# Performance work log

Hardware: AMD Instinct MI355X
Metric: run time of the kernel (lower is better)

## Reference

```python
import jax, jax.numpy as jnp
import numpy as np

B, N, DIM, HEADS = 1, 4096, 1024, 16
HEAD_DIM = DIM // HEADS
SCALE = HEAD_DIM ** -0.5
GRID = 64  # GRID*GRID == N, power-of-2 Hilbert grid


def _hilbert_d2xy(n, d):
    # standard Hilbert curve distance->(x,y), vectorized in numpy
    rx = np.zeros_like(d)
    ry = np.zeros_like(d)
    x = np.zeros_like(d)
    y = np.zeros_like(d)
    t = d.copy()
    s = 1
    while s < n:
        rx = (t // 2) & 1
        ry = (t ^ rx) & 1
        # rotate
        swap = ry == 0
        flip = swap & (rx == 1)
        x_f = np.where(flip, s - 1 - x, x)
        y_f = np.where(flip, s - 1 - y, y)
        x, y = np.where(swap, y_f, x_f), np.where(swap, x_f, y_f)
        x = x + s * rx
        y = y + s * ry
        t = t // 4
        s *= 2
    return x, y


def _hilbert_indices(n_tokens, grid):
    d = np.arange(n_tokens)
    hx, hy = _hilbert_d2xy(grid, d)
    # token at Hilbert distance d lives at row-major position hy*grid+hx
    return (hy * grid + hx).astype(np.int32)


def setup_inputs() -> dict:
    key = jax.random.key(0)
    k1, k2, k3 = jax.random.split(key, 3)
    x = jax.random.normal(k1, (B, N, DIM), dtype=jnp.float32)
    w_qkv = jax.random.normal(k2, (3 * DIM, DIM), dtype=jnp.float32) * (DIM ** -0.5)
    w_out = jax.random.normal(k3, (DIM, DIM), dtype=jnp.float32) * (DIM ** -0.5)
    indices = jnp.asarray(_hilbert_indices(N, GRID))
    return {"x": x, "w_qkv": w_qkv, "w_out": w_out, "indices": indices}


def reference(x, w_qkv, w_out, indices):
    b, n, c = x.shape
    # qkv projection: nn.Linear -> x @ W^T, reshape to [B,N,3,H,Dh]
    qkv = jnp.einsum("bnc,dc->bnd", x, w_qkv).reshape(b, n, 3, HEADS, HEAD_DIM)
    q, k, v = qkv[:, :, 0], qkv[:, :, 1], qkv[:, :, 2]  # each [B,N,H,Dh]
    # Hilbert gather along sequence
    q = q[:, indices]
    k = k[:, indices]
    v = v[:, indices]
    # full softmax attention per head
    scores = jnp.einsum("bnhd,bmhd->bhnm", q, k) * SCALE
    attn = jax.nn.softmax(scores, axis=-1)
    out = jnp.einsum("bhnm,bmhd->bnhd", attn, v)  # [B,N,H,Dh]
    # scatter back to original order
    inv = jnp.argsort(indices)
    out = out[:, inv].reshape(b, n, c)
    return jnp.einsum("bnc,dc->bnd", out, w_out)
```

## Files before the change

kernel.cpp:

```cpp
#include <hip/hip_runtime.h>
#include <stdint.h>

#define NTOK 4096
#define HD 64
#define DIMC 1024

typedef __attribute__((ext_vector_type(8))) short s16x8;
typedef __attribute__((ext_vector_type(4))) float f32x4;

#if __has_builtin(__builtin_amdgcn_exp2f)
#define EXP2(x) __builtin_amdgcn_exp2f(x)
#else
#define EXP2(x) exp2f(x)
#endif

__device__ inline unsigned short f2bf(float f) {
  union { float f; unsigned u; } v; v.f = f;
  unsigned r = v.u + 0x7FFFu + ((v.u >> 16) & 1u);
  return (unsigned short)(r >> 16);
}

__device__ inline unsigned cvt_pk_bf16(float lo, float hi) {
  unsigned r;
  asm("v_cvt_pk_bf16_f32 %0, %1, %2" : "=v"(r) : "v"(lo), "v"(hi));
  return r;
}

__device__ inline float bf2f(unsigned short u) {
  union { unsigned u; float f; } v; v.u = ((unsigned)u) << 16;
  return v.f;
}

__device__ inline void gld16(const void* g, void* s) {
  __builtin_amdgcn_global_load_lds((const __attribute__((address_space(1))) void*)g,
                                   (__attribute__((address_space(3))) void*)s, 16, 0, 0);
}

#define N4_X   1048576
#define N4_WQ  786432
#define N4_WO  262144
__global__ void cvt_all(const float4* __restrict__ x, const float4* __restrict__ wq,
                        const float4* __restrict__ wo, ushort4* __restrict__ xb,
                        ushort4* __restrict__ wqb, ushort4* __restrict__ wob) {
  int i = blockIdx.x * 256 + threadIdx.x;
  const float4* s; ushort4* d; int off;
  if (i < N4_X) { s = x; d = xb; off = i; }
  else if (i < N4_X + N4_WQ) { s = wq; d = wqb; off = i - N4_X; }
  else { s = wo; d = wob; off = i - (N4_X + N4_WQ); }
  float4 v = s[off];
  ushort4 o;
  o.x = f2bf(v.x); o.y = f2bf(v.y); o.z = f2bf(v.z); o.w = f2bf(v.w);
  d[off] = o;
}

#define QSCALE 0.18033688011112042f
template<int EPI>
__global__ __launch_bounds__(256) void gemm_bt(
    const unsigned short* __restrict__ A,
    const unsigned short* __restrict__ B,
    float* __restrict__ outf,
    unsigned short* __restrict__ qb,
    unsigned short* __restrict__ kb,
    unsigned short* __restrict__ vtb,
    int K, int Nout)
{
  __shared__ unsigned short As[128 * 32];
  __shared__ unsigned short Bs[128 * 32];
  const int t = threadIdx.x;
  const int l = t & 63;
  const int w = t >> 6;
  const int wr = w >> 1, wc = w & 1;
  const int bm = blockIdx.x, bn = blockIdx.y;

  f32x4 acc[4][4];
#pragma unroll
  for (int m = 0; m < 4; ++m)
#pragma unroll
    for (int n = 0; n < 4; ++n)
#pragma unroll
      for (int r = 0; r < 4; ++r) acc[m][n][r] = 0.f;

  for (int kt = 0; kt < K; kt += 32) {
    __syncthreads();
#pragma unroll
    for (int j = 0; j < 2; ++j) {
      const int o = j * 4096 + t * 16;
      const int row = o >> 6;
      const int cole = (o & 63) >> 1;
      gld16(A + (size_t)(bm * 128 + row) * K + kt + cole, (char*)As + o);
      gld16(B + (size_t)(bn * 128 + row) * K + kt + cole, (char*)Bs + o);
    }
    __syncthreads();
    s16x8 af[4], bfr[4];
    const int cb = (l >> 4) * 16;
#pragma unroll
    for (int m = 0; m < 4; ++m)
      af[m] = *(const s16x8*)((const char*)As + (wr * 64 + m * 16 + (l & 15)) * 64 + cb);
#pragma unroll
    for (int n = 0; n < 4; ++n)
      bfr[n] = *(const s16x8*)((const char*)Bs + (wc * 64 + n * 16 + (l & 15)) * 64 + cb);
#pragma unroll
    for (int m = 0; m < 4; ++m)
#pragma unroll
      for (int n = 0; n < 4; ++n)
        acc[m][n] = __builtin_amdgcn_mfma_f32_16x16x32_bf16(af[m], bfr[n], acc[m][n], 0, 0, 0);
  }

#pragma unroll
  for (int m = 0; m < 4; ++m) {
#pragma unroll
    for (int n = 0; n < 4; ++n) {
#pragma unroll
      for (int r = 0; r < 4; ++r) {
        const int gm = bm * 128 + wr * 64 + m * 16 + (l >> 4) * 4 + r;
        const int gn = bn * 128 + wc * 64 + n * 16 + (l & 15);
        const float val = acc[m][n][r];
        if (EPI == 0) {
          const int part = gn >> 10;
          const int h = (gn >> 6) & 15;
          const int dd = gn & 63;
          if (part == 0)      qb[((size_t)h * NTOK + gm) * HD + dd] = f2bf(val * QSCALE);
          else if (part == 1) kb[((size_t)h * NTOK + gm) * HD + dd] = f2bf(val);
          else                vtb[((size_t)h * HD + dd) * NTOK + gm] = f2bf(val);
        } else {
          outf[(size_t)gm * Nout + gn] = val;
        }
      }
    }
  }
}

__global__ __launch_bounds__(128, 4) void fa_split(
    const unsigned short* __restrict__ Q,
    const unsigned short* __restrict__ Kin,
    const unsigned short* __restrict__ Vt,
    unsigned short* __restrict__ Opart,
    float* __restrict__ Lpart)
{
  __shared__ unsigned short Ks[2][32 * 64];
  __shared__ unsigned short Vs[2][64 * 32];

  const int t = threadIdx.x, l = t & 63, w = t >> 6;
  const int g = l >> 4, q = l & 15;
  const int wg = blockIdx.x;
  const int h = wg & 15;
  const int qt = (wg >> 4) & 63;
  const int half = wg >> 10;
  const int q0 = qt * 64 + w * 32;
  const int kbase0 = half * (NTOK / 2);
  const unsigned short* Qh = Q + (size_t)h * NTOK * HD;
  const unsigned short* Kh = Kin + (size_t)h * NTOK * HD;
  const unsigned short* Vh = Vt + (size_t)h * HD * NTOK;

  int offK[2], offV[2];
#pragma unroll
  for (int j = 0; j < 2; ++j) {
    const int o = j * 2048 + t * 16;
    const int rho = o >> 7;
    const int c = o & 127;
    const int n = ((rho & 12) << 1) | ((rho & 16) >> 2) | (rho & 3);
    offK[j] = n * 128 + (c ^ ((rho & 7) << 4));
    const int rv = o >> 6;
    offV[j] = rv * (NTOK * 2) + (o & 63);
  }

  s16x8 qf[2][2];
#pragma unroll
  for (int rb = 0; rb < 2; ++rb)
#pragma unroll
    for (int tq = 0; tq < 2; ++tq)
      qf[rb][tq] = *(const s16x8*)(Qh + (size_t)(q0 + rb * 16 + q) * HD + tq * 32 + g * 8);

  s16x8 ones;
#pragma unroll
  for (int i = 0; i < 8; ++i) ones[i] = (short)0x3F80;

  f32x4 oacc[2][4], lacc[2];
#pragma unroll
  for (int rb = 0; rb < 2; ++rb) {
#pragma unroll
    for (int db = 0; db < 4; ++db)
#pragma unroll
      for (int r = 0; r < 4; ++r) oacc[rb][db][r] = 0.f;
#pragma unroll
    for (int r = 0; r < 4; ++r) lacc[rb][r] = 0.f;
  }

#pragma unroll
  for (int j = 0; j < 2; ++j) {
    const int o = j * 2048 + t * 16;
    gld16((const char*)Kh + (size_t)kbase0 * 128 + offK[j], (char*)Ks[0] + o);
    gld16((const char*)Vh + (size_t)kbase0 * 2 + offV[j], (char*)Vs[0] + o);
  }
  __syncthreads();

  int cur = 0;
  const int NIT = (NTOK / 2) / 32;
  for (int it = 0; it < NIT; ++it) {
    if (it + 1 < NIT) {
      const char* kp = (const char*)Kh + (size_t)(kbase0 + (it + 1) * 32) * 128;
      const char* vp = (const char*)Vh + (size_t)(kbase0 + (it + 1) * 32) * 2;
#pragma unroll
      for (int j = 0; j < 2; ++j) {
        const int o = j * 2048 + t * 16;
        gld16(kp + offK[j], (char*)Ks[cur ^ 1] + o);
        gld16(vp + offV[j], (char*)Vs[cur ^ 1] + o);
      }
    }

    const char* kb = (const char*)Ks[cur];
    const char* vb = (const char*)Vs[cur];

    f32x4 sc[2][2];
    __builtin_amdgcn_s_setprio(1);
#pragma unroll
    for (int kb2 = 0; kb2 < 2; ++kb2) {
      const int row = kb2 * 16 + q;
      const int swz = (row & 7) << 4;
      s16x8 kf0 = *(const s16x8*)(kb + row * 128 + ((g * 16) ^ swz));
      s16x8 kf1 = *(const s16x8*)(kb + row * 128 + ((64 + g * 16) ^ swz));
#pragma unroll
      for (int rb = 0; rb < 2; ++rb) {
        f32x4 z = {0.f, 0.f, 0.f, 0.f};
        z = __builtin_amdgcn_mfma_f32_16x16x32_bf16(kf0, qf[rb][0], z, 0, 0, 0);
        sc[rb][kb2] = __builtin_amdgcn_mfma_f32_16x16x32_bf16(kf1, qf[rb][1], z, 0, 0, 0);
      }
    }
    __builtin_amdgcn_s_setprio(0);

    union PU { unsigned u[4]; s16x8 v; } pu[2];
#pragma unroll
    for (int rb = 0; rb < 2; ++rb) {
      pu[rb].u[0] = cvt_pk_bf16(EXP2(sc[rb][0][0]), EXP2(sc[rb][0][1]));
      pu[rb].u[1] = cvt_pk_bf16(EXP2(sc[rb][0][2]), EXP2(sc[rb][0][3]));
      pu[rb].u[2] = cvt_pk_bf16(EXP2(sc[rb][1][0]), EXP2(sc[rb][1][1]));
      pu[rb].u[3] = cvt_pk_bf16(EXP2(sc[rb][1][2]), EXP2(sc[rb][1][3]));
    }

    __builtin_amdgcn_s_setprio(1);
#pragma unroll
    for (int db = 0; db < 4; ++db) {
      const int row = db * 16 + q;
      s16x8 vf = *(const s16x8*)(vb + row * 64 + g * 16);
#pragma unroll
      for (int rb = 0; rb < 2; ++rb)
        oacc[rb][db] = __builtin_amdgcn_mfma_f32_16x16x32_bf16(vf, pu[rb].v, oacc[rb][db], 0, 0, 0);
    }
#pragma unroll
    for (int rb = 0; rb < 2; ++rb)
      lacc[rb] = __builtin_amdgcn_mfma_f32_16x16x32_bf16(ones, pu[rb].v, lacc[rb], 0, 0, 0);
    __builtin_amdgcn_s_setprio(0);

    __syncthreads();
    cur ^= 1;
  }

  const size_t pbase = ((size_t)(half * 16 + h) * NTOK);
#pragma unroll
  for (int rb = 0; rb < 2; ++rb) {
    const int nn = q0 + rb * 16 + q;
#pragma unroll
    for (int db = 0; db < 4; ++db) {
      uint2 pr;
      pr.x = cvt_pk_bf16(oacc[rb][db][0], oacc[rb][db][1]);
      pr.y = cvt_pk_bf16(oacc[rb][db][2], oacc[rb][db][3]);
      *(uint2*)(Opart + (pbase + nn) * HD + db * 16 + g * 4) = pr;
    }
    if (g == 0) Lpart[pbase + nn] = lacc[rb][0];
  }
}

__global__ __launch_bounds__(256) void fa_combine(
    const unsigned short* __restrict__ Opart,
    const float* __restrict__ Lpart,
    unsigned short* __restrict__ O)
{
  const int tid = blockIdx.x * 256 + threadIdx.x;
  const int d4 = tid & 15;
  const int n = (tid >> 4) & 4095;
  const int h = tid >> 16;
  const size_t e0 = ((size_t)h * NTOK + n) * HD + d4 * 4;
  const size_t e1 = e0 + (size_t)16 * NTOK * HD;
  ushort4 a = *(const ushort4*)(Opart + e0);
  ushort4 b = *(const ushort4*)(Opart + e1);
  const float inv = 1.f / (Lpart[(size_t)h * NTOK + n] + Lpart[(size_t)(16 + h) * NTOK + n]);
  ushort4 o;
  o.x = f2bf((bf2f(a.x) + bf2f(b.x)) * inv);
  o.y = f2bf((bf2f(a.y) + bf2f(b.y)) * inv);
  o.z = f2bf((bf2f(a.z) + bf2f(b.z)) * inv);
  o.w = f2bf((bf2f(a.w) + bf2f(b.w)) * inv);
  *(ushort4*)(O + (size_t)n * DIMC + h * HD + d4 * 4) = o;
}

extern "C" void kernel_launch(void* const* d_in, const int* in_sizes, int n_in,
                              void* d_out, int out_size, void* d_ws, size_t ws_size,
                              hipStream_t stream) {
  const float* x    = (const float*)d_in[0];
  const float* wqkv = (const float*)d_in[1];
  const float* wout = (const float*)d_in[2];
  float* out = (float*)d_out;
  char* ws = (char*)d_ws;

  unsigned short* xb    = (unsigned short*)(ws);
  unsigned short* wqkvb = (unsigned short*)(ws + 8388608);
  unsigned short* Qb    = (unsigned short*)(ws + 16777216);
  unsigned short* Kb    = (unsigned short*)(ws + 25165824);
  unsigned short* Vtb   = (unsigned short*)(ws + 33554432);
  unsigned short* aob   = (unsigned short*)(ws + 41943040);
  unsigned short* woutb = (unsigned short*)(ws + 50331648);
  float*          Lp    = (float*)(ws + 52428800);
  unsigned short* Opart = (unsigned short*)(ws);

  cvt_all<<<8192, 256, 0, stream>>>((const float4*)x, (const float4*)wqkv, (const float4*)wout,
                                    (ushort4*)xb, (ushort4*)wqkvb, (ushort4*)woutb);

  gemm_bt<0><<<dim3(32, 24), 256, 0, stream>>>(xb, wqkvb, nullptr, Qb, Kb, Vtb, 1024, 3072);

  fa_split<<<2048, 128, 0, stream>>>(Qb, Kb, Vtb, Opart, Lp);

  fa_combine<<<4096, 256, 0, stream>>>(Opart, Lp, aob);

  gemm_bt<1><<<dim3(32, 8), 256, 0, stream>>>(aob, woutb, out, nullptr, nullptr, nullptr, 1024, 1024);
}
```

Measured before the change: 167.9 us.

## Fuse split-attention combine into output projection GEMM and swizzle V tile LDS

Removes the separate fa_combine kernel. The output GEMM now loads the two partial attention outputs and their softmax denominators, normalizes them, and writes the bf16 A tile straight into LDS. This saves one kernel launch and the round trip of the combined activation through global memory. The A-tile loads are now synchronous vector loads with per-element arithmetic instead of async global-to-LDS copies, which may stall the GEMM mainloop. Separately, it adds an XOR swizzle to the V tile layout in LDS within the attention kernel to cut bank conflicts, and it repacks the workspace offsets.

```diff
diff --git a/kernel.cpp b/kernel.cpp
--- a/kernel.cpp
+++ b/kernel.cpp
@@ -54,15 +54,12 @@
 }
 
 #define QSCALE 0.18033688011112042f
-template<int EPI>
-__global__ __launch_bounds__(256) void gemm_bt(
+__global__ __launch_bounds__(256) void gemm_qkv(
     const unsigned short* __restrict__ A,
     const unsigned short* __restrict__ B,
-    float* __restrict__ outf,
     unsigned short* __restrict__ qb,
     unsigned short* __restrict__ kb,
-    unsigned short* __restrict__ vtb,
-    int K, int Nout)
+    unsigned short* __restrict__ vtb)
 {
   __shared__ unsigned short As[128 * 32];
   __shared__ unsigned short Bs[128 * 32];
@@ -71,6 +68,7 @@
   const int w = t >> 6;
   const int wr = w >> 1, wc = w & 1;
   const int bm = blockIdx.x, bn = blockIdx.y;
+  const int K = 1024;
 
   f32x4 acc[4][4];
 #pragma unroll
@@ -115,16 +113,12 @@
         const int gm = bm * 128 + wr * 64 + m * 16 + (l >> 4) * 4 + r;
         const int gn = bn * 128 + wc * 64 + n * 16 + (l & 15);
         const float val = acc[m][n][r];
-        if (EPI == 0) {
-          const int part = gn >> 10;
-          const int h = (gn >> 6) & 15;
-          const int dd = gn & 63;
-          if (part == 0)      qb[((size_t)h * NTOK + gm) * HD + dd] = f2bf(val * QSCALE);
-          else if (part == 1) kb[((size_t)h * NTOK + gm) * HD + dd] = f2bf(val);
-          else                vtb[((size_t)h * HD + dd) * NTOK + gm] = f2bf(val);
-        } else {
-          outf[(size_t)gm * Nout + gn] = val;
-        }
+        const int part = gn >> 10;
+        const int h = (gn >> 6) & 15;
+        const int dd = gn & 63;
+        if (part == 0)      qb[((size_t)h * NTOK + gm) * HD + dd] = f2bf(val * QSCALE);
+        else if (part == 1) kb[((size_t)h * NTOK + gm) * HD + dd] = f2bf(val);
+        else                vtb[((size_t)h * HD + dd) * NTOK + gm] = f2bf(val);
       }
     }
   }
@@ -161,7 +155,8 @@
     const int n = ((rho & 12) << 1) | ((rho & 16) >> 2) | (rho & 3);
     offK[j] = n * 128 + (c ^ ((rho & 7) << 4));
     const int rv = o >> 6;
-    offV[j] = rv * (NTOK * 2) + (o & 63);
+    const int cv = o & 63;
+    offV[j] = rv * (NTOK * 2) + (cv ^ (((rv >> 1) & 3) << 4));
   }
 
   s16x8 qf[2][2];
@@ -238,10 +233,11 @@
     }
 
     __builtin_amdgcn_s_setprio(1);
+    const int vswz = ((q >> 1) & 3) << 4;
 #pragma unroll
     for (int db = 0; db < 4; ++db) {
       const int row = db * 16 + q;
-      s16x8 vf = *(const s16x8*)(vb + row * 64 + g * 16);
+      s16x8 vf = *(const s16x8*)(vb + row * 64 + ((g * 16) ^ vswz));
 #pragma unroll
       for (int rb = 0; rb < 2; ++rb)
         oacc[rb][db] = __builtin_amdgcn_mfma_f32_16x16x32_bf16(vf, pu[rb].v, oacc[rb][db], 0, 0, 0);
@@ -270,26 +266,77 @@
   }
 }
 
-__global__ __launch_bounds__(256) void fa_combine(
+__global__ __launch_bounds__(256) void gemm_out(
     const unsigned short* __restrict__ Opart,
     const float* __restrict__ Lpart,
-    unsigned short* __restrict__ O)
+    const unsigned short* __restrict__ Bw,
+    float* __restrict__ outf)
 {
-  const int tid = blockIdx.x * 256 + threadIdx.x;
-  const int d4 = tid & 15;
-  const int n = (tid >> 4) & 4095;
-  const int h = tid >> 16;
-  const size_t e0 = ((size_t)h * NTOK + n) * HD + d4 * 4;
-  const size_t e1 = e0 + (size_t)16 * NTOK * HD;
-  ushort4 a = *(const ushort4*)(Opart + e0);
-  ushort4 b = *(const ushort4*)(Opart + e1);
-  const float inv = 1.f / (Lpart[(size_t)h * NTOK + n] + Lpart[(size_t)(16 + h) * NTOK + n]);
-  ushort4 o;
-  o.x = f2bf((bf2f(a.x) + bf2f(b.x)) * inv);
-  o.y = f2bf((bf2f(a.y) + bf2f(b.y)) * inv);
-  o.z = f2bf((bf2f(a.z) + bf2f(b.z)) * inv);
-  o.w = f2bf((bf2f(a.w) + bf2f(b.w)) * inv);
-  *(ushort4*)(O + (size_t)n * DIMC + h * HD + d4 * 4) = o;
+  __shared__ unsigned short As[128 * 32];
+  __shared__ unsigned short Bs[128 * 32];
+  const int t = threadIdx.x;
+  const int l = t & 63;
+  const int w = t >> 6;
+  const int wr = w >> 1, wc = w & 1;
+  const int bm = blockIdx.x, bn = blockIdx.y;
+
+  f32x4 acc[4][4];
+#pragma unroll
+  for (int m = 0; m < 4; ++m)
+#pragma unroll
+    for (int n = 0; n < 4; ++n)
+#pragma unroll
+      for (int r = 0; r < 4; ++r) acc[m][n][r] = 0.f;
+
+  for (int kt = 0; kt < 1024; kt += 32) {
+    __syncthreads();
+#pragma unroll
+    for (int j = 0; j < 2; ++j) {
+      const int o = j * 4096 + t * 16;
+      const int row = o >> 6;
+      const int cole = (o & 63) >> 1;
+      gld16(Bw + (size_t)(bn * 128 + row) * 1024 + kt + cole, (char*)Bs + o);
+      const int kg = kt + cole;
+      const int hh = kg >> 6, dd = kg & 63;
+      const int mm = bm * 128 + row;
+      const size_t base = ((size_t)hh * NTOK + mm) * HD + dd;
+      s16x8 p0 = *(const s16x8*)(Opart + base);
+      s16x8 p1 = *(const s16x8*)(Opart + base + (size_t)16 * NTOK * HD);
+      const float inv = 1.f / (Lpart[(size_t)hh * NTOK + mm] +
+                               Lpart[(size_t)16 * NTOK + (size_t)hh * NTOK + mm]);
+      union PA { unsigned u[4]; s16x8 v; } pa;
+#pragma unroll
+      for (int e = 0; e < 4; ++e)
+        pa.u[e] = cvt_pk_bf16((bf2f((unsigned short)p0[2 * e]) + bf2f((unsigned short)p1[2 * e])) * inv,
+                              (bf2f((unsigned short)p0[2 * e + 1]) + bf2f((unsigned short)p1[2 * e + 1])) * inv);
+      *(s16x8*)((char*)As + o) = pa.v;
+    }
+    __syncthreads();
+    s16x8 af[4], bfr[4];
+    const int cb = (l >> 4) * 16;
+#pragma unroll
+    for (int m = 0; m < 4; ++m)
+      af[m] = *(const s16x8*)((const char*)As + (wr * 64 + m * 16 + (l & 15)) * 64 + cb);
+#pragma unroll
+    for (int n = 0; n < 4; ++n)
+      bfr[n] = *(const s16x8*)((const char*)Bs + (wc * 64 + n * 16 + (l & 15)) * 64 + cb);
+#pragma unroll
+    for (int m = 0; m < 4; ++m)
+#pragma unroll
+      for (int n = 0; n < 4; ++n)
+        acc[m][n] = __builtin_amdgcn_mfma_f32_16x16x32_bf16(af[m], bfr[n], acc[m][n], 0, 0, 0);
+  }
+
+#pragma unroll
+  for (int m = 0; m < 4; ++m)
+#pragma unroll
+    for (int n = 0; n < 4; ++n)
+#pragma unroll
+      for (int r = 0; r < 4; ++r) {
+        const int gm = bm * 128 + wr * 64 + m * 16 + (l >> 4) * 4 + r;
+        const int gn = bn * 128 + wc * 64 + n * 16 + (l & 15);
+        outf[(size_t)gm * 1024 + gn] = acc[m][n][r];
+      }
 }
 
 extern "C" void kernel_launch(void* const* d_in, const int* in_sizes, int n_in,
@@ -301,24 +348,21 @@
   float* out = (float*)d_out;
   char* ws = (char*)d_ws;
 
+  unsigned short* Opart = (unsigned short*)(ws);
   unsigned short* xb    = (unsigned short*)(ws);
   unsigned short* wqkvb = (unsigned short*)(ws + 8388608);
-  unsigned short* Qb    = (unsigned short*)(ws + 16777216);
-  unsigned short* Kb    = (unsigned short*)(ws + 25165824);
-  unsigned short* Vtb   = (unsigned short*)(ws + 33554432);
-  unsigned short* aob   = (unsigned short*)(ws + 41943040);
-  unsigned short* woutb = (unsigned short*)(ws + 50331648);
-  float*          Lp    = (float*)(ws + 52428800);
-  unsigned short* Opart = (unsigned short*)(ws);
+  float*          Lp    = (float*)(ws + 16777216);
+  unsigned short* Qb    = (unsigned short*)(ws + 17825792);
+  unsigned short* Kb    = (unsigned short*)(ws + 26214400);
+  unsigned short* Vtb   = (unsigned short*)(ws + 34603008);
+  unsigned short* woutb = (unsigned short*)(ws + 42991616);
 
   cvt_all<<<8192, 256, 0, stream>>>((const float4*)x, (const float4*)wqkv, (const float4*)wout,
                                     (ushort4*)xb, (ushort4*)wqkvb, (ushort4*)woutb);
 
-  gemm_bt<0><<<dim3(32, 24), 256, 0, stream>>>(xb, wqkvb, nullptr, Qb, Kb, Vtb, 1024, 3072);
+  gemm_qkv<<<dim3(32, 24), 256, 0, stream>>>(xb, wqkvb, Qb, Kb, Vtb);
 
   fa_split<<<2048, 128, 0, stream>>>(Qb, Kb, Vtb, Opart, Lp);
 
-  fa_combine<<<4096, 256, 0, stream>>>(Opart, Lp, aob);
-
-  gemm_bt<1><<<dim3(32, 8), 256, 0, stream>>>(aob, woutb, out, nullptr, nullptr, nullptr, 1024, 1024);
-}
+  gemm_out<<<dim3(32, 8), 256, 0, stream>>>(Opart, Lp, woutb, out);
+}
```

New measurement: 170.3 us. About the same (+1.4%).
